# Performance work log

Hardware: AMD Instinct MI355X
Metric: run time of the kernel (lower is better)

Reference implementation:

```python
import jax, jax.numpy as jnp
import numpy as np

HIDDEN = 1024
HEADS = 16
HEAD_DIM = HIDDEN // HEADS


def setup_inputs() -> dict:
    key = jax.random.key(0)
    k0, k1, k2, k3, k4 = jax.random.split(key, 5)
    s = 0.02
    return {
        "data": jax.random.normal(k0, (4, 2048, HIDDEN), dtype=jnp.float32),
        "qkv_w": jax.random.normal(k1, (3 * HIDDEN, HIDDEN), dtype=jnp.float32) * s,  # (out,in) torch layout
        "qkv_b": jax.random.normal(k2, (3 * HIDDEN,), dtype=jnp.float32) * s,
        "out_w": jax.random.normal(k3, (HIDDEN, HIDDEN), dtype=jnp.float32) * s,
        "out_b": jax.random.normal(k4, (HIDDEN,), dtype=jnp.float32) * s,
    }


def reference(data, qkv_w, qkv_b, out_w, out_b):
    B, T, C = data.shape
    qkv = jnp.einsum("btc,oc->bto", data, qkv_w) + qkv_b  # [B,T,3C]
    q, k, v = jnp.split(qkv, 3, axis=2)
    # [B,T,C] -> [B,H,T,D]
    def heads(x):
        return x.reshape(B, T, HEADS, HEAD_DIM).transpose(0, 2, 1, 3)
    q, k, v = heads(q), heads(k), heads(v)
    scale = 1.0 / jnp.sqrt(jnp.float32(HEAD_DIM))
    att = jnp.einsum("bhqd,bhkd->bhqk", q, k) * scale  # [B,H,T,T]
    causal = jnp.tril(jnp.ones((T, T), dtype=bool))
    att = jnp.where(causal[None, None, :, :], att, -jnp.inf)
    att = jax.nn.softmax(att, axis=-1)
    out = jnp.einsum("bhqk,bhkd->bhqd", att, v)  # [B,H,T,D]
    out = out.transpose(0, 2, 1, 3).reshape(B, T, C)
    return jnp.einsum("btc,oc->bto", out, out_w) + out_b
```

## Files before the change

### kernel.cpp

```cpp
#include <hip/hip_runtime.h>
#include <hip/hip_bf16.h>
#include <stdint.h>

typedef __attribute__((ext_vector_type(8))) __bf16 bf16x8;
typedef __attribute__((ext_vector_type(4))) float f32x4;
typedef __attribute__((ext_vector_type(16))) float f32x16;
typedef __attribute__((ext_vector_type(4))) unsigned int u32x4;

#define HIDDEN 1024
#define HEADS 16
#define HD 64
#define NB 4
#define T_ 2048
#define M_ROWS (NB * T_)
#define SCL2 0.18033688f
#define FIXM 32.0f

__device__ __forceinline__ unsigned short f2bf(float x) {
  unsigned u = __builtin_bit_cast(unsigned, x);
  u += 0x7fff + ((u >> 16) & 1);
  return (unsigned short)(u >> 16);
}

__device__ __forceinline__ unsigned pk2(float a, float b) {
  unsigned ua = __builtin_bit_cast(unsigned, a) + 0x8000u;
  unsigned ub = __builtin_bit_cast(unsigned, b) + 0x8000u;
  return __builtin_amdgcn_perm(ub, ua, 0x07060302);
}

__device__ __forceinline__ f32x4 mfma16(bf16x8 a, bf16x8 b, f32x4 c) {
  return __builtin_amdgcn_mfma_f32_16x16x32_bf16(a, b, c, 0, 0, 0);
}
__device__ __forceinline__ f32x16 mfma32(bf16x8 a, bf16x8 b, f32x16 c) {
  return __builtin_amdgcn_mfma_f32_32x32x16_bf16(a, b, c, 0, 0, 0);
}

__device__ __forceinline__ void lds16(const void* g, void* l) {
  __builtin_amdgcn_global_load_lds(
      (const __attribute__((address_space(1))) unsigned int*)g,
      (__attribute__((address_space(3))) unsigned int*)l, 16, 0, 0);
}

__device__ __forceinline__ bf16x8 ldg8(const unsigned short* p) {
  return __builtin_bit_cast(bf16x8, *(const u32x4*)p);
}

__global__ void cvt_bf16(const float* __restrict__ in,
                         unsigned short* __restrict__ out, int n4) {
  int i = blockIdx.x * blockDim.x + threadIdx.x;
  int stride = gridDim.x * blockDim.x;
  for (; i < n4; i += stride) {
    float4 v = ((const float4*)in)[i];
    ushort4 o;
    o.x = f2bf(v.x); o.y = f2bf(v.y); o.z = f2bf(v.z); o.w = f2bf(v.w);
    ((ushort4*)out)[i] = o;
  }
}


#define RD(BUF, OFF) \
  __builtin_bit_cast(bf16x8, *(const u32x4*)((BUF) + (OFF)))

template <int EPI, int NT>
__global__ __launch_bounds__(512, 4) void gemm8(
    const unsigned short* __restrict__ A, const unsigned short* __restrict__ Bm,
    const float* __restrict__ bias, unsigned short* __restrict__ Qb,
    unsigned short* __restrict__ Kb, unsigned short* __restrict__ Vtb,
    float* __restrict__ Cf) {
  constexpr int K = 1024;
  constexpr int N = NT * 256;
  __shared__ __align__(16) char LB[3][24576];
  const int tid = threadIdx.x;
  const int wv = tid >> 6, lane = tid & 63;
  const int l16 = lane & 15, grp = lane >> 4;
  const int wm = wv >> 2, wn = wv & 3;
  const int bid = blockIdx.x;
  const int sw = (bid & 7) * ((64 * NT) >> 3) + (bid >> 3);
  const int by = sw / NT, bx = sw % NT;
  const int brow0 = by * 128, bcol0 = bx * 256;

  const int ua = (tid & 7) ^ ((tid >> 3) & 7);
  const unsigned short* aptr =
      A + (size_t)(brow0 + (tid >> 3) * 2 + (ua >> 2)) * K + (ua & 3) * 8;
  const unsigned short* bptr =
      Bm + (size_t)(bcol0 + (tid >> 3) * 2 + (ua >> 2)) * K + (ua & 3) * 8;

  const int swu = ((((l16 & 1) * 4) + grp) ^ ((l16 >> 1) & 7)) * 16;
  const int aoff = (wm * 32 + (l16 >> 1)) * 128 + swu;
  const int boff = 8192 + (wn * 32 + (l16 >> 1)) * 128 + swu;

#define STAGE(c, t)                                                   \
  do {                                                                \
    lds16(aptr + (size_t)(t) * 32, (char*)LB[c] + wv * 1024);         \
    lds16(bptr + (size_t)(t) * 32, (char*)LB[c] + 8192 + wv * 1024);  \
    lds16(bptr + (size_t)128 * K + (size_t)(t) * 32,                  \
          (char*)LB[c] + 16384 + wv * 1024);                          \
  } while (0)

  f32x4 acc[4][4];
#pragma unroll
  for (int m = 0; m < 4; m++)
#pragma unroll
    for (int n = 0; n < 4; n++) acc[m][n] = (f32x4){0.f, 0.f, 0.f, 0.f};

  STAGE(0, 0);
  STAGE(1, 1);
  asm volatile("s_waitcnt vmcnt(3)" ::: "memory");
  __builtin_amdgcn_sched_barrier(0);
  __builtin_amdgcn_s_barrier();

  int c = 0, c2 = 2;
#pragma unroll 1
  for (int t = 0; t < 32; ++t) {
    const char* buf = (const char*)LB[c];
    bf16x8 bf[4], af[4];
#pragma unroll
    for (int n = 0; n < 4; n++) bf[n] = RD(buf, boff + n * 1024);
#pragma unroll
    for (int m = 0; m < 4; m++) af[m] = RD(buf, aoff + m * 1024);
    if (t < 30) STAGE(c2, t + 2);
    __builtin_amdgcn_s_barrier();
    __builtin_amdgcn_s_setprio(1);
#pragma unroll
    for (int m = 0; m < 4; m++)
#pragma unroll
      for (int n = 0; n < 4; n++) acc[m][n] = mfma16(af[m], bf[n], acc[m][n]);
    __builtin_amdgcn_s_setprio(0);
    if (t < 30) {
      asm volatile("s_waitcnt vmcnt(3)" ::: "memory");
      __builtin_amdgcn_sched_barrier(0);
    } else if (t == 30) {
      asm volatile("s_waitcnt vmcnt(0)" ::: "memory");
      __builtin_amdgcn_sched_barrier(0);
    }
    if (t < 31) __builtin_amdgcn_s_barrier();
    c = (c == 2) ? 0 : c + 1;
    c2 = (c2 == 2) ? 0 : c2 + 1;
  }

#pragma unroll
  for (int m = 0; m < 4; m++) {
#pragma unroll
    for (int n = 0; n < 4; n++) {
      int col = bcol0 + wn * 64 + n * 16 + l16;
      int row0 = brow0 + wm * 64 + m * 16 + grp * 4;
      float bs = bias[col];
      if (EPI == 0) {
        int part = col >> 10, rem = col & 1023;
        int h = rem >> 6, d = rem & 63;
#pragma unroll
        for (int r = 0; r < 4; r++) {
          int rw = row0 + r;
          int b = rw >> 11, t = rw & 2047;
          unsigned short val = f2bf(acc[m][n][r] + bs);
          size_t bh = (size_t)(b * 16 + h);
          if (part == 0)
            Qb[(bh * T_ + t) * HD + d] = val;
          else if (part == 1)
            Kb[(bh * T_ + t) * HD + d] = val;
          else {
            int k = t & 31;
            int rr = (k & 3) + 4 * (k >> 3);
            int s = (rr & 7) + 8 * ((k >> 2) & 1) + 16 * (rr >> 3);
            Vtb[(bh * HD + d) * T_ + (t & ~31) + s] = val;
          }
        }
      } else {
#pragma unroll
        for (int r = 0; r < 4; r++)
          Cf[(size_t)(row0 + r) * N + col] = acc[m][n][r] + bs;
      }
    }
  }
#undef STAGE
}

__global__ __launch_bounds__(256, 3) void attn32(
    const unsigned short* __restrict__ Q, const unsigned short* __restrict__ K,
    const unsigned short* __restrict__ Vt, unsigned short* __restrict__ Ao) {
  __shared__ __align__(16) unsigned short Kl[2][32 * 64];
  __shared__ __align__(16) unsigned short Vl[2][32 * 64];
  const int i = blockIdx.x;
  const int bh = i & 63;
  const int g = (i < 512) ? (15 - (i >> 6)) : ((i - 512) >> 6);
  const int wv = threadIdx.x >> 6, lane = threadIdx.x & 63;
  const int l31 = lane & 31, hi = lane >> 5;
  const int qt = g * 4 + wv;
  const int maxqt = g * 4 + 3;
  const unsigned short* Qh = Q + (size_t)bh * T_ * HD;
  const unsigned short* Kh = K + (size_t)bh * T_ * HD;
  const unsigned short* Vh = Vt + (size_t)bh * HD * T_;
  const int b_ = bh >> 4, h_ = bh & 15;

  const int sj = threadIdx.x >> 3, su = threadIdx.x & 7;
  const int sup = su ^ (sj & 7);
  const unsigned short* ksrc = Kh + sj * HD + sup * 8;
  const unsigned short* vsrc =
      Vh + (size_t)(sj + 32 * (sup >> 2)) * T_ + (sup & 3) * 8;
  char* kdst0 = (char*)&Kl[0][0] + wv * 1024;
  char* kdst1 = (char*)&Kl[1][0] + wv * 1024;
  char* vdst0 = (char*)&Vl[0][0] + wv * 1024;
  char* vdst1 = (char*)&Vl[1][0] + wv * 1024;

#define STAGE(B, KC)                                     \
  do {                                                   \
    int kt_ = (KC) * 32;                                 \
    lds16(ksrc + (size_t)kt_ * HD, (B) ? kdst1 : kdst0); \
    lds16(vsrc + kt_, (B) ? vdst1 : vdst0);              \
  } while (0)

  int rdoff[4];
#pragma unroll
  for (int ks = 0; ks < 4; ks++)
    rdoff[ks] = l31 * 128 + (((2 * ks + hi) ^ (l31 & 7)) << 4);

  bf16x8 qf[4];
  const int qbase = qt * 32;
#pragma unroll
  for (int st = 0; st < 4; st++)
    qf[st] = ldg8(&Qh[(size_t)(qbase + l31) * HD + st * 16 + hi * 8]);

  f32x16 o0, o1;
#pragma unroll
  for (int r = 0; r < 16; r++) { o0[r] = 0.f; o1[r] = 0.f; }
  float rl = 0.f;

#define CHUNK(B, MASKED)                                                     \
  do {                                                                       \
    const char* kb = (const char*)&Kl[(B)][0];                               \
    const char* vb = (const char*)&Vl[(B)][0];                               \
    bf16x8 KF[4], VF[4];                                                     \
    _Pragma("unroll") for (int ks = 0; ks < 4; ks++) {                       \
      KF[ks] = __builtin_bit_cast(bf16x8, *(const u32x4*)(kb + rdoff[ks]));  \
      VF[ks] = __builtin_bit_cast(bf16x8, *(const u32x4*)(vb + rdoff[ks]));  \
    }                                                                        \
    f32x16 sa;                                                               \
    _Pragma("unroll") for (int r = 0; r < 16; r++) sa[r] = 0.f;              \
    sa = mfma32(KF[0], qf[0], sa);                                           \
    sa = mfma32(KF[1], qf[1], sa);                                           \
    sa = mfma32(KF[2], qf[2], sa);                                           \
    sa = mfma32(KF[3], qf[3], sa);                                           \
    float pv[16];                                                            \
    _Pragma("unroll") for (int r = 0; r < 16; r++) {                         \
      float arg = __builtin_fmaf(sa[r], SCL2, -FIXM);                        \
      if (MASKED) {                                                          \
        int key = (r & 3) + 8 * (r >> 2) + 4 * hi;                           \
        if (key > l31) arg = -1e30f;                                         \
      }                                                                      \
      pv[r] = exp2f(arg);                                                    \
      rl += pv[r];                                                           \
    }                                                                        \
    u32x4 pa0u, pa1u;                                                        \
    pa0u.x = pk2(pv[0], pv[1]);                                              \
    pa0u.y = pk2(pv[2], pv[3]);                                              \
    pa0u.z = pk2(pv[4], pv[5]);                                              \
    pa0u.w = pk2(pv[6], pv[7]);                                              \
    pa1u.x = pk2(pv[8], pv[9]);                                              \
    pa1u.y = pk2(pv[10], pv[11]);                                            \
    pa1u.z = pk2(pv[12], pv[13]);                                            \
    pa1u.w = pk2(pv[14], pv[15]);                                            \
    bf16x8 pa0 = __builtin_bit_cast(bf16x8, pa0u);                           \
    bf16x8 pa1 = __builtin_bit_cast(bf16x8, pa1u);                           \
    o0 = mfma32(VF[0], pa0, o0);                                             \
    o0 = mfma32(VF[1], pa1, o0);                                             \
    o1 = mfma32(VF[2], pa0, o1);                                             \
    o1 = mfma32(VF[3], pa1, o1);                                             \
  } while (0)

  STAGE(0, 0);
  __syncthreads();
  int cur = 0;
  for (int kc = 0; kc <= maxqt; kc++) {
    if (kc < maxqt) STAGE(cur ^ 1, kc + 1);
    if (kc < qt) {
      CHUNK(cur, 0);
    } else if (kc == qt) {
      CHUNK(cur, 1);
    }
    __syncthreads();
    cur ^= 1;
  }

  float rlt = rl + __shfl_xor(rl, 32);
  float inv = 1.f / rlt;
  const size_t base =
      ((size_t)b_ * T_ + qbase + l31) * HIDDEN + h_ * HD + hi * 4;
#pragma unroll
  for (int gg = 0; gg < 4; gg++) {
    uint2 u;
    u.x = pk2(o0[4 * gg] * inv, o0[4 * gg + 1] * inv);
    u.y = pk2(o0[4 * gg + 2] * inv, o0[4 * gg + 3] * inv);
    *(uint2*)&Ao[base + gg * 8] = u;
  }
#pragma unroll
  for (int gg = 0; gg < 4; gg++) {
    uint2 u;
    u.x = pk2(o1[4 * gg] * inv, o1[4 * gg + 1] * inv);
    u.y = pk2(o1[4 * gg + 2] * inv, o1[4 * gg + 3] * inv);
    *(uint2*)&Ao[base + 32 + gg * 8] = u;
  }
#undef STAGE
#undef CHUNK
}

extern "C" void kernel_launch(void* const* d_in, const int* in_sizes, int n_in,
                              void* d_out, int out_size, void* d_ws,
                              size_t ws_size, hipStream_t stream) {
  const float* data = (const float*)d_in[0];
  const float* qkvw = (const float*)d_in[1];
  const float* qkvb = (const float*)d_in[2];
  const float* outw = (const float*)d_in[3];
  const float* outb = (const float*)d_in[4];
  float* out = (float*)d_out;
  char* ws = (char*)d_ws;

  unsigned short* dataBf = (unsigned short*)(ws);
  unsigned short* qkvwBf = (unsigned short*)(ws + 16777216);
  unsigned short* outwBf = (unsigned short*)(ws + 23068672);
  unsigned short* Qb = (unsigned short*)(ws + 25165824);
  unsigned short* Kb = (unsigned short*)(ws + 41943040);
  unsigned short* Vtb = (unsigned short*)(ws + 58720256);
  unsigned short* attnO = dataBf;

  cvt_bf16<<<2048, 256, 0, stream>>>(data, dataBf, (M_ROWS * HIDDEN) / 4);
  cvt_bf16<<<1024, 256, 0, stream>>>(qkvw, qkvwBf, (3 * HIDDEN * HIDDEN) / 4);
  cvt_bf16<<<512, 256, 0, stream>>>(outw, outwBf, (HIDDEN * HIDDEN) / 4);

  gemm8<0, 12><<<768, 512, 0, stream>>>(dataBf, qkvwBf, qkvb, Qb, Kb, Vtb,
                                        nullptr);
  attn32<<<1024, 256, 0, stream>>>(Qb, Kb, Vtb, attnO);
  gemm8<1, 4><<<256, 512, 0, stream>>>(attnO, outwBf, outb, nullptr, nullptr,
                                       nullptr, out);
}
```

Baseline: 198.3 us.

## Fuse conversion launches, reshape GEMM tiles, and double K/V chunk size in attention

```diff
diff --git a/kernel.cpp b/kernel.cpp
--- a/kernel.cpp
+++ b/kernel.cpp
@@ -45,15 +45,29 @@
   return __builtin_bit_cast(bf16x8, *(const u32x4*)p);
 }
 
-__global__ void cvt_bf16(const float* __restrict__ in,
-                         unsigned short* __restrict__ out, int n4) {
+__global__ void cvt3(const float* __restrict__ i0, unsigned short* __restrict__ o0,
+                     int n0, const float* __restrict__ i1,
+                     unsigned short* __restrict__ o1, int n1,
+                     const float* __restrict__ i2,
+                     unsigned short* __restrict__ o2, int n2) {
   int i = blockIdx.x * blockDim.x + threadIdx.x;
   int stride = gridDim.x * blockDim.x;
-  for (; i < n4; i += stride) {
-    float4 v = ((const float4*)in)[i];
+  int tot = n0 + n1 + n2;
+  for (; i < tot; i += stride) {
+    const float* src;
+    unsigned short* dst;
+    int j = i;
+    if (j < n0) {
+      src = i0; dst = o0;
+    } else if ((j -= n0) < n1) {
+      src = i1; dst = o1;
+    } else {
+      j -= n1; src = i2; dst = o2;
+    }
+    float4 v = ((const float4*)src)[j];
     ushort4 o;
     o.x = f2bf(v.x); o.y = f2bf(v.y); o.z = f2bf(v.z); o.w = f2bf(v.w);
-    ((ushort4*)out)[i] = o;
+    ((ushort4*)dst)[j] = o;
   }
 }
 
@@ -62,22 +76,24 @@
   __builtin_bit_cast(bf16x8, *(const u32x4*)((BUF) + (OFF)))
 
 template <int EPI, int NT>
-__global__ __launch_bounds__(512, 4) void gemm8(
+__global__ __launch_bounds__(512, 6) void gemm8(
     const unsigned short* __restrict__ A, const unsigned short* __restrict__ Bm,
     const float* __restrict__ bias, unsigned short* __restrict__ Qb,
     unsigned short* __restrict__ Kb, unsigned short* __restrict__ Vtb,
     float* __restrict__ Cf) {
   constexpr int K = 1024;
-  constexpr int N = NT * 256;
-  __shared__ __align__(16) char LB[3][24576];
+  constexpr int N = NT * 128;
+  __shared__ __align__(16) char LB[2][24576];
   const int tid = threadIdx.x;
   const int wv = tid >> 6, lane = tid & 63;
   const int l16 = lane & 15, grp = lane >> 4;
-  const int wm = wv >> 2, wn = wv & 3;
+  const int wm = wv >> 1, wn = wv & 1;
   const int bid = blockIdx.x;
-  const int sw = (bid & 7) * ((64 * NT) >> 3) + (bid >> 3);
-  const int by = sw / NT, bx = sw % NT;
-  const int brow0 = by * 128, bcol0 = bx * 256;
+  const int xcd = bid & 7, l = bid >> 3;
+  const int g2 = l >> 5, il = l & 31;
+  const int by = xcd * 4 + (il & 3);
+  const int bx = g2 * 8 + (il >> 2);
+  const int brow0 = by * 256, bcol0 = bx * 128;
 
   const int ua = (tid & 7) ^ ((tid >> 3) & 7);
   const unsigned short* aptr =
@@ -87,14 +103,14 @@
 
   const int swu = ((((l16 & 1) * 4) + grp) ^ ((l16 >> 1) & 7)) * 16;
   const int aoff = (wm * 32 + (l16 >> 1)) * 128 + swu;
-  const int boff = 8192 + (wn * 32 + (l16 >> 1)) * 128 + swu;
-
-#define STAGE(c, t)                                                   \
-  do {                                                                \
-    lds16(aptr + (size_t)(t) * 32, (char*)LB[c] + wv * 1024);         \
-    lds16(bptr + (size_t)(t) * 32, (char*)LB[c] + 8192 + wv * 1024);  \
-    lds16(bptr + (size_t)128 * K + (size_t)(t) * 32,                  \
-          (char*)LB[c] + 16384 + wv * 1024);                          \
+  const int boff = 16384 + (wn * 32 + (l16 >> 1)) * 128 + swu;
+
+#define STAGE(c, t)                                                     \
+  do {                                                                  \
+    lds16(aptr + (size_t)(t) * 32, (char*)LB[c] + wv * 1024);           \
+    lds16(aptr + (size_t)128 * K + (size_t)(t) * 32,                    \
+          (char*)LB[c] + 8192 + wv * 1024);                             \
+    lds16(bptr + (size_t)(t) * 32, (char*)LB[c] + 16384 + wv * 1024);   \
   } while (0)
 
   f32x4 acc[4][4];
@@ -104,38 +120,31 @@
     for (int n = 0; n < 4; n++) acc[m][n] = (f32x4){0.f, 0.f, 0.f, 0.f};
 
   STAGE(0, 0);
-  STAGE(1, 1);
-  asm volatile("s_waitcnt vmcnt(3)" ::: "memory");
+  asm volatile("s_waitcnt vmcnt(0)" ::: "memory");
   __builtin_amdgcn_sched_barrier(0);
   __builtin_amdgcn_s_barrier();
 
-  int c = 0, c2 = 2;
 #pragma unroll 1
   for (int t = 0; t < 32; ++t) {
-    const char* buf = (const char*)LB[c];
+    const int cb = t & 1;
+    if (t < 31) STAGE(cb ^ 1, t + 1);
+    const char* buf = (const char*)LB[cb];
     bf16x8 bf[4], af[4];
 #pragma unroll
     for (int n = 0; n < 4; n++) bf[n] = RD(buf, boff + n * 1024);
 #pragma unroll
     for (int m = 0; m < 4; m++) af[m] = RD(buf, aoff + m * 1024);
-    if (t < 30) STAGE(c2, t + 2);
-    __builtin_amdgcn_s_barrier();
     __builtin_amdgcn_s_setprio(1);
 #pragma unroll
     for (int m = 0; m < 4; m++)
 #pragma unroll
       for (int n = 0; n < 4; n++) acc[m][n] = mfma16(af[m], bf[n], acc[m][n]);
     __builtin_amdgcn_s_setprio(0);
-    if (t < 30) {
-      asm volatile("s_waitcnt vmcnt(3)" ::: "memory");
-      __builtin_amdgcn_sched_barrier(0);
-    } else if (t == 30) {
+    if (t < 31) {
       asm volatile("s_waitcnt vmcnt(0)" ::: "memory");
       __builtin_amdgcn_sched_barrier(0);
+      __builtin_amdgcn_s_barrier();
     }
-    if (t < 31) __builtin_amdgcn_s_barrier();
-    c = (c == 2) ? 0 : c + 1;
-    c2 = (c2 == 2) ? 0 : c2 + 1;
   }
 
 #pragma unroll
@@ -178,15 +187,15 @@
 __global__ __launch_bounds__(256, 3) void attn32(
     const unsigned short* __restrict__ Q, const unsigned short* __restrict__ K,
     const unsigned short* __restrict__ Vt, unsigned short* __restrict__ Ao) {
-  __shared__ __align__(16) unsigned short Kl[2][32 * 64];
-  __shared__ __align__(16) unsigned short Vl[2][32 * 64];
+  __shared__ __align__(16) unsigned short Kl[2][64 * 64];
+  __shared__ __align__(16) unsigned short Vl[2][64 * 64];
   const int i = blockIdx.x;
   const int bh = i & 63;
   const int g = (i < 512) ? (15 - (i >> 6)) : ((i - 512) >> 6);
   const int wv = threadIdx.x >> 6, lane = threadIdx.x & 63;
   const int l31 = lane & 31, hi = lane >> 5;
   const int qt = g * 4 + wv;
-  const int maxqt = g * 4 + 3;
+  const int kmax = g * 2 + 1;
   const unsigned short* Qh = Q + (size_t)bh * T_ * HD;
   const unsigned short* Kh = K + (size_t)bh * T_ * HD;
   const unsigned short* Vh = Vt + (size_t)bh * HD * T_;
@@ -197,16 +206,16 @@
   const unsigned short* ksrc = Kh + sj * HD + sup * 8;
   const unsigned short* vsrc =
       Vh + (size_t)(sj + 32 * (sup >> 2)) * T_ + (sup & 3) * 8;
-  char* kdst0 = (char*)&Kl[0][0] + wv * 1024;
-  char* kdst1 = (char*)&Kl[1][0] + wv * 1024;
-  char* vdst0 = (char*)&Vl[0][0] + wv * 1024;
-  char* vdst1 = (char*)&Vl[1][0] + wv * 1024;
-
-#define STAGE(B, KC)                                     \
-  do {                                                   \
-    int kt_ = (KC) * 32;                                 \
-    lds16(ksrc + (size_t)kt_ * HD, (B) ? kdst1 : kdst0); \
-    lds16(vsrc + kt_, (B) ? vdst1 : vdst0);              \
+
+#define STAGE(B, C2)                                                      \
+  do {                                                                    \
+    int kt_ = (C2) * 64;                                                  \
+    char* kd = (char*)&Kl[(B)][0] + wv * 1024;                            \
+    char* vd = (char*)&Vl[(B)][0] + wv * 1024;                            \
+    lds16(ksrc + (size_t)kt_ * HD, kd);                                   \
+    lds16(ksrc + (size_t)(kt_ + 32) * HD, kd + 4096);                     \
+    lds16(vsrc + kt_, vd);                                                \
+    lds16(vsrc + kt_ + 32, vd + 4096);                                    \
   } while (0)
 
   int rdoff[4];
@@ -225,10 +234,10 @@
   for (int r = 0; r < 16; r++) { o0[r] = 0.f; o1[r] = 0.f; }
   float rl = 0.f;
 
-#define CHUNK(B, MASKED)                                                     \
+#define CHUNKH(B, H, MASKED)                                                 \
   do {                                                                       \
-    const char* kb = (const char*)&Kl[(B)][0];                               \
-    const char* vb = (const char*)&Vl[(B)][0];                               \
+    const char* kb = (const char*)&Kl[(B)][0] + (H) * 4096;                  \
+    const char* vb = (const char*)&Vl[(B)][0] + (H) * 4096;                  \
     bf16x8 KF[4], VF[4];                                                     \
     _Pragma("unroll") for (int ks = 0; ks < 4; ks++) {                       \
       KF[ks] = __builtin_bit_cast(bf16x8, *(const u32x4*)(kb + rdoff[ks]));  \
@@ -270,12 +279,19 @@
   STAGE(0, 0);
   __syncthreads();
   int cur = 0;
-  for (int kc = 0; kc <= maxqt; kc++) {
-    if (kc < maxqt) STAGE(cur ^ 1, kc + 1);
-    if (kc < qt) {
-      CHUNK(cur, 0);
-    } else if (kc == qt) {
-      CHUNK(cur, 1);
+  const int halfq = qt >> 1, oddq = qt & 1;
+  for (int kc2 = 0; kc2 <= kmax; kc2++) {
+    if (kc2 < kmax) STAGE(cur ^ 1, kc2 + 1);
+    if (kc2 < halfq) {
+      CHUNKH(cur, 0, 0);
+      CHUNKH(cur, 1, 0);
+    } else if (kc2 == halfq) {
+      if (oddq) {
+        CHUNKH(cur, 0, 0);
+        CHUNKH(cur, 1, 1);
+      } else {
+        CHUNKH(cur, 0, 1);
+      }
     }
     __syncthreads();
     cur ^= 1;
@@ -300,7 +316,7 @@
     *(uint2*)&Ao[base + 32 + gg * 8] = u;
   }
 #undef STAGE
-#undef CHUNK
+#undef CHUNKH
 }
 
 extern "C" void kernel_launch(void* const* d_in, const int* in_sizes, int n_in,
@@ -322,13 +338,13 @@
   unsigned short* Vtb = (unsigned short*)(ws + 58720256);
   unsigned short* attnO = dataBf;
 
-  cvt_bf16<<<2048, 256, 0, stream>>>(data, dataBf, (M_ROWS * HIDDEN) / 4);
-  cvt_bf16<<<1024, 256, 0, stream>>>(qkvw, qkvwBf, (3 * HIDDEN * HIDDEN) / 4);
-  cvt_bf16<<<512, 256, 0, stream>>>(outw, outwBf, (HIDDEN * HIDDEN) / 4);
-
-  gemm8<0, 12><<<768, 512, 0, stream>>>(dataBf, qkvwBf, qkvb, Qb, Kb, Vtb,
+  cvt3<<<2048, 256, 0, stream>>>(data, dataBf, (M_ROWS * HIDDEN) / 4, qkvw,
+                                 qkvwBf, (3 * HIDDEN * HIDDEN) / 4, outw,
+                                 outwBf, (HIDDEN * HIDDEN) / 4);
+
+  gemm8<0, 24><<<768, 512, 0, stream>>>(dataBf, qkvwBf, qkvb, Qb, Kb, Vtb,
                                         nullptr);
   attn32<<<1024, 256, 0, stream>>>(Qb, Kb, Vtb, attnO);
-  gemm8<1, 4><<<256, 512, 0, stream>>>(attnO, outwBf, outb, nullptr, nullptr,
+  gemm8<1, 8><<<256, 512, 0, stream>>>(attnO, outwBf, outb, nullptr, nullptr,
                                        nullptr, out);
 }
```

Result: slower. 636.4 us (+220.9%).
